# Performance work log

Hardware: AMD Instinct MI355X
Metric: run time of the kernel (lower is better)

## Reference

```python
import jax, jax.numpy as jnp
import numpy as np

LEAK = 0.2
N, C, T, H, DOUT = 512, 16, 15, 32, 32


def setup_inputs() -> dict:
    key = jax.random.key(0)
    k = jax.random.split(key, 5)
    x = jax.random.normal(k[0], (N, C), dtype=jnp.float32)
    adj = jax.random.uniform(k[1], (N, N, T), dtype=jnp.float32)
    W1 = jax.random.normal(k[2], (2 * C, T + 1, H), dtype=jnp.float32) * 0.05
    W2 = jax.random.normal(k[3], (2 * C, T + 1, DOUT), dtype=jnp.float32) * 0.05
    W3 = jax.random.normal(k[4], (C, H), dtype=jnp.float32) * 0.05
    return {"x": x, "adj": adj, "W1": W1, "W2": W2, "W3": W3}


def reference(x, adj, W1, W2, W3):
    n, c = x.shape
    # input_diag: [N,N,C,1], diagonal copy of node features
    diag = jnp.einsum('mn,ni->mni', jnp.eye(n, dtype=x.dtype), x)[..., None]
    # D = concat(adj-weighted broadcast of x, diag) along edge-type axis -> [N,N,C,T+1]
    D = jnp.concatenate([jnp.einsum('mnt,ni->mnit', adj, x), diag], axis=3)
    # symmetrize along channel axis -> [N,N,2C,T+1]
    D = jnp.concatenate([D, jnp.transpose(D, (1, 0, 2, 3))], axis=2)
    K = jnp.einsum('mnit,ith->mnh', D, W1)   # [N,N,H]
    V = jnp.einsum('mnit,itd->mnd', D, W2)   # [N,N,DOUT]
    Q = x @ W3                               # [N,H]
    logits1 = jnp.einsum('nh,nmh->nm', Q, K)
    logits2 = jnp.einsum('mh,nmh->nm', Q, K)
    s1 = jax.nn.softmax(logits1, axis=1)
    s2 = jax.nn.softmax(logits2, axis=0)
    temp = jnp.einsum('nm,nmd->nd', s1, V) + jnp.einsum('nm,nmd->md', s2, V)
    return jnp.maximum(temp, LEAK * temp)  # lrelu
```

## Files before the change

kernel.cpp:

```cpp
#include <hip/hip_runtime.h>
#include <hip/hip_bf16.h>

#define NNODE 512
#define CCH   16
#define TT    15
#define TP    16
#define HH    32
#define DD    32

typedef unsigned short u16;
typedef unsigned int   u32;
typedef short bf8 __attribute__((ext_vector_type(8)));
typedef float f4  __attribute__((ext_vector_type(4)));

__device__ __forceinline__ float bf2f(u16 v) {
    union { u32 u; float f; } x; x.u = ((u32)v) << 16; return x.f;
}
__device__ __forceinline__ u16 f2bf(float f) {
    union { float f; u32 u; } x; x.f = f;
    u32 u = x.u;
    return (u16)((u + 0x7FFFu + ((u >> 16) & 1u)) >> 16);
}
__device__ __forceinline__ void unpack8(uint4 p, float* o) {
    o[0]=bf2f((u16)(p.x & 0xffffu)); o[1]=bf2f((u16)(p.x >> 16));
    o[2]=bf2f((u16)(p.y & 0xffffu)); o[3]=bf2f((u16)(p.y >> 16));
    o[4]=bf2f((u16)(p.z & 0xffffu)); o[5]=bf2f((u16)(p.z >> 16));
    o[6]=bf2f((u16)(p.w & 0xffffu)); o[7]=bf2f((u16)(p.w >> 16));
}
__device__ __forceinline__ uint4 pack8(const u16* v) {
    return make_uint4((u32)v[0]|((u32)v[1]<<16), (u32)v[2]|((u32)v[3]<<16),
                      (u32)v[4]|((u32)v[5]<<16), (u32)v[6]|((u32)v[7]<<16));
}

__global__ __launch_bounds__(256) void k_prep_adjp(
    const float* __restrict__ x, const float* __restrict__ W1,
    const float* __restrict__ W2, const float* __restrict__ W3,
    const float* __restrict__ adj,
    u16* __restrict__ A1, u16* __restrict__ B1,
    u16* __restrict__ A2, u16* __restrict__ B2,
    u16* __restrict__ Qb, float* __restrict__ QAd, float* __restrict__ QB,
    u16* __restrict__ adjP, u16* __restrict__ adjPT)
{
    int tid = threadIdx.x;
    if (blockIdx.x < 512) {
        int n = blockIdx.x;
        __shared__ alignas(16) float xs[CCH];
        __shared__ alignas(16) float A1row[512], B1row[512];
        __shared__ alignas(16) float Qs[HH];
        if (tid < CCH) xs[tid] = x[n*CCH + tid];
        __syncthreads();
        float xr[CCH];
        #pragma unroll
        for (int i=0;i<CCH;i++) xr[i]=xs[i];
        #pragma unroll
        for (int rep=0; rep<2; rep++) {
            int c = tid + rep*256;
            float a1=0.f,b1=0.f,a2=0.f,b2=0.f;
            #pragma unroll
            for (int i=0;i<CCH;i++) {
                a1 += xr[i]*W1[i*512 + c];
                b1 += xr[i]*W1[(CCH+i)*512 + c];
                a2 += xr[i]*W2[i*512 + c];
                b2 += xr[i]*W2[(CCH+i)*512 + c];
            }
            A1[(size_t)n*512 + c]=f2bf(a1); B1[(size_t)n*512 + c]=f2bf(b1);
            A2[(size_t)n*512 + c]=f2bf(a2); B2[(size_t)n*512 + c]=f2bf(b2);
            A1row[c]=a1; B1row[c]=b1;
        }
        if (tid < HH) {
            float q=0.f;
            #pragma unroll
            for (int i=0;i<CCH;i++) q += xr[i]*W3[i*HH + tid];
            Qs[tid]=q; Qb[(size_t)n*HH + tid]=f2bf(q);
        }
        __syncthreads();
        if (tid < TP) {
            float qa=0.f, qb=0.f;
            #pragma unroll
            for (int h=0;h<HH;h++) { qa += Qs[h]*A1row[tid*HH+h]; qb += Qs[h]*B1row[tid*HH+h]; }
            QAd[(size_t)n*TP + tid]=qa; QB[(size_t)n*TP + tid]=qb;
        }
    } else {
        int b = blockIdx.x - 512;
        int n0 = (b >> 4) * 32, m0 = (b & 15) * 32;
        __shared__ alignas(16) u16 s[32*520];
        #pragma unroll
        for (int i = 0; i < 60; i++) {
            int e = tid + i*256;
            int nl = e / 480; int rem = e - nl*480;
            int ml = rem / 15; int t = rem - ml*15;
            float v = adj[((size_t)(n0+nl)*512 + (m0+ml))*TT + t];
            s[nl*520 + ml*16 + t] = f2bf(v);
        }
        #pragma unroll
        for (int i = 0; i < 4; i++) {
            int e = tid + i*256; int nl = e >> 5, ml = e & 31;
            s[nl*520 + ml*16 + 15] = ((n0+nl) == (m0+ml)) ? (u16)0x3F80 : (u16)0;
        }
        __syncthreads();
        #pragma unroll
        for (int i = 0; i < 8; i++) {
            int c = tid + i*256;
            int nl = c >> 6, off = (c & 63) * 8;
            uint4 vv = *(const uint4*)(s + nl*520 + off);
            *(uint4*)(adjP + (size_t)(n0+nl)*8192 + m0*16 + off) = vv;
        }
        #pragma unroll
        for (int i = 0; i < 8; i++) {
            int c = tid + i*256;
            int ml = c >> 6, nlh = c & 63, nl = nlh >> 1, half = nlh & 1;
            uint4 vv = *(const uint4*)(s + nl*520 + ml*16 + half*8);
            *(uint4*)(adjPT + (size_t)(m0+ml)*8192 + (n0+nl)*16 + half*8) = vv;
        }
    }
}

__global__ __launch_bounds__(256) void k_gemmGH(
    const u16* __restrict__ Qb, const u16* __restrict__ A1, const u16* __restrict__ B1,
    const u16* __restrict__ A2, const u16* __restrict__ B2,
    u16* __restrict__ G, u16* __restrict__ H,
    u16* __restrict__ A2T, u16* __restrict__ B2T)
{
    int tid = threadIdx.x;
    int bx = blockIdx.x;
    if (bx < 8192) {
        int wv = tid >> 6, lane = tid & 63;
        int l15 = lane & 15, quad = lane >> 4;
        bool isH = bx >= 4096;
        int w = ((isH ? bx - 4096 : bx) << 2) + wv;
        int rt = w >> 9;
        int ct = w & 511;
        const u16* Bsrc = isH ? B1 : A1;
        u16* Dst = isH ? H : G;
        bf8 afrag = *(const bf8*)(Qb + (size_t)(rt*16 + l15)*32 + quad*8);
        bf8 bfrag = *(const bf8*)(Bsrc + (size_t)ct*512 + l15*32 + quad*8);
        f4 acc = {0.f, 0.f, 0.f, 0.f};
        acc = __builtin_amdgcn_mfma_f32_16x16x32_bf16(afrag, bfrag, acc, 0, 0, 0);
        #pragma unroll
        for (int r = 0; r < 4; r++)
            Dst[(size_t)(rt*16 + quad*4 + r)*8192 + ct*16 + l15] = f2bf(acc[r]);
    } else {
        int b = bx - 8192;
        bool isB = b >= 64;
        const u16* src = isB ? B2 : A2;
        u16* dst = isB ? B2T : A2T;
        int idx = ((b & 63) << 8) + tid;
        int d = idx >> 9, k = idx & 511;
        u16 tmp[16];
        #pragma unroll
        for (int t = 0; t < 16; t++) tmp[t] = src[(size_t)k*512 + t*32 + d];
        uint4* o = (uint4*)(dst + (size_t)d*8192 + k*16);
        o[0] = pack8(tmp); o[1] = pack8(tmp+8);
    }
}

__global__ __launch_bounds__(256) void k_combine(
    const u16* __restrict__ adjP, const u16* __restrict__ adjPT,
    const u16* __restrict__ G, const u16* __restrict__ H,
    const float* __restrict__ QAd, const float* __restrict__ QB,
    float* __restrict__ L1, float* __restrict__ L2T)
{
    int m0 = blockIdx.x*16, n0 = blockIdx.y*16;
    int tid = threadIdx.x, ml = tid & 15, nl = tid >> 4;
    int n = n0 + nl, m = m0 + ml;
    __shared__ alignas(16) float tr[16*17];
    const uint4* pA = (const uint4*)(adjP  + (size_t)n*8192 + m*16);
    const uint4* pT = (const uint4*)(adjPT + (size_t)n*8192 + m*16);
    const uint4* pG = (const uint4*)(G + (size_t)n*8192 + m*16);
    const uint4* pH = (const uint4*)(H + (size_t)m*8192 + n*16);
    float a[16], at[16], g[16], h[16], qa[16], qb[16];
    unpack8(pA[0], a);  unpack8(pA[1], a+8);
    unpack8(pT[0], at); unpack8(pT[1], at+8);
    unpack8(pG[0], g);  unpack8(pG[1], g+8);
    unpack8(pH[0], h);  unpack8(pH[1], h+8);
    #pragma unroll
    for (int q4 = 0; q4 < 4; q4++) {
        float4 va = *(const float4*)(QAd + m*16 + q4*4);
        float4 vb = *(const float4*)(QB  + n*16 + q4*4);
        qa[q4*4+0]=va.x; qa[q4*4+1]=va.y; qa[q4*4+2]=va.z; qa[q4*4+3]=va.w;
        qb[q4*4+0]=vb.x; qb[q4*4+1]=vb.y; qb[q4*4+2]=vb.z; qb[q4*4+3]=vb.w;
    }
    float l1 = 0.f, l2 = 0.f;
    #pragma unroll
    for (int t = 0; t < 16; t++) {
        l1 = fmaf(a[t], g[t],  fmaf(at[t], qb[t], l1));
        l2 = fmaf(a[t], qa[t], fmaf(at[t], h[t],  l2));
    }
    L1[(size_t)n*NNODE + m] = l1;
    tr[ml*17+nl] = l2;
    __syncthreads();
    int r = tid >> 4, c = tid & 15;
    L2T[(size_t)(m0+r)*NNODE + n0+c] = tr[r*17+c];
}

__global__ __launch_bounds__(256) void k_softmax_w(
    const float* __restrict__ L1, const float* __restrict__ L2T,
    const u16* __restrict__ adjP, const u16* __restrict__ adjPT,
    u16* __restrict__ W1c, u16* __restrict__ W2c,
    float* __restrict__ u1, float* __restrict__ v2)
{
    int b = blockIdx.x, tid = threadIdx.x;
    bool first = b < NNODE;
    int j = first ? b : b - NNODE;
    const float* row = first ? (L1 + (size_t)j*NNODE) : (L2T + (size_t)j*NNODE);
    u16* W  = (first ? W1c : W2c) + (size_t)j*8192;
    float* uv = (first ? u1 : v2) + (size_t)j*TP;

    float v0 = row[tid], v1 = row[tid+256];
    float mx = fmaxf(v0, v1);
    #pragma unroll
    for (int o=32; o; o>>=1) mx = fmaxf(mx, __shfl_xor(mx, o, 64));
    __shared__ alignas(16) float red[4], red2[4], ur[4][16];
    int lane = tid & 63, wv = tid >> 6;
    if (!lane) red[wv] = mx;
    __syncthreads();
    mx = fmaxf(fmaxf(red[0],red[1]), fmaxf(red[2],red[3]));
    float e0 = __expf(v0 - mx), e1 = __expf(v1 - mx);
    float sm = e0 + e1;
    #pragma unroll
    for (int o=32; o; o>>=1) sm += __shfl_xor(sm, o, 64);
    if (!lane) red2[wv] = sm;
    __syncthreads();
    float inv = 1.0f / (red2[0]+red2[1]+red2[2]+red2[3]);
    float sa = e0*inv, sb = e1*inv;

    const u16* ap = adjP  + (size_t)j*8192;
    const u16* tp = adjPT + (size_t)j*8192;
    float u[16];
    #pragma unroll
    for (int t=0;t<16;t++) u[t]=0.f;
    #pragma unroll
    for (int half = 0; half < 2; half++) {
        int k = tid + half*256;
        float sv = half ? sb : sa;
        const uint4* p = (const uint4*)(ap + k*16);
        float av[16]; unpack8(p[0], av); unpack8(p[1], av+8);
        u16 o16[16];
        #pragma unroll
        for (int t=0;t<16;t++) o16[t] = f2bf(sv*av[t]);
        uint4* wp = (uint4*)(W + k*16);
        wp[0] = pack8(o16); wp[1] = pack8(o16+8);
        const uint4* q = (const uint4*)(tp + k*16);
        float tv[16]; unpack8(q[0], tv); unpack8(q[1], tv+8);
        #pragma unroll
        for (int t=0;t<16;t++) u[t] = fmaf(sv, tv[t], u[t]);
    }
    #pragma unroll
    for (int t=0;t<16;t++) {
        #pragma unroll
        for (int o=32; o; o>>=1) u[t] += __shfl_xor(u[t], o, 64);
    }
    if (!lane) {
        #pragma unroll
        for (int t=0;t<16;t++) ur[wv][t] = u[t];
    }
    __syncthreads();
    if (tid < 16) uv[tid] = ur[0][tid]+ur[1][tid]+ur[2][tid]+ur[3][tid];
}

__global__ __launch_bounds__(256) void k_gemm2(
    const u16* __restrict__ W1c, const u16* __restrict__ W2c,
    const u16* __restrict__ A2T, const u16* __restrict__ B2T,
    float* __restrict__ tempP)
{
    int tid = threadIdx.x;
    int wv = tid >> 6, lane = tid & 63, l15 = lane & 15, quad = lane >> 4;
    int w = blockIdx.x*4 + wv;
    int kc = w & 15, dt = (w >> 4) & 1, jt = w >> 5;
    size_t aRow = (size_t)(jt*16 + l15)*8192;
    size_t bRow = (size_t)(dt*16 + l15)*8192;
    int kt0 = kc*512 + quad*8;
    f4 acc = {0.f, 0.f, 0.f, 0.f};
    #pragma unroll
    for (int s = 0; s < 16; s++) {
        int kt = kt0 + s*32;
        bf8 aw1 = *(const bf8*)(W1c + aRow + kt);
        bf8 ba2 = *(const bf8*)(A2T + bRow + kt);
        acc = __builtin_amdgcn_mfma_f32_16x16x32_bf16(aw1, ba2, acc, 0, 0, 0);
        bf8 aw2 = *(const bf8*)(W2c + aRow + kt);
        bf8 bb2 = *(const bf8*)(B2T + bRow + kt);
        acc = __builtin_amdgcn_mfma_f32_16x16x32_bf16(aw2, bb2, acc, 0, 0, 0);
    }
    #pragma unroll
    for (int r = 0; r < 4; r++)
        tempP[((size_t)kc*NNODE + jt*16 + quad*4 + r)*DD + dt*16 + l15] = acc[r];
}

__global__ __launch_bounds__(256) void k_final(
    const float* __restrict__ tempP, const float* __restrict__ u1, const float* __restrict__ v2,
    const u16* __restrict__ A2, const u16* __restrict__ B2, float* __restrict__ out)
{
    int j0 = blockIdx.x * 8;
    int tid = threadIdx.x;
    int j = tid >> 5, d = tid & 31;
    int jj = j0 + j;
    float acc = 0.f;
    #pragma unroll
    for (int kc=0;kc<16;kc++) acc += tempP[((size_t)kc*NNODE + jj)*DD + d];
    #pragma unroll
    for (int t=0;t<TP;t++) {
        acc += u1[(size_t)jj*TP + t] * bf2f(B2[(size_t)jj*512 + t*32 + d]);
        acc += v2[(size_t)jj*TP + t] * bf2f(A2[(size_t)jj*512 + t*32 + d]);
    }
    out[(size_t)jj*DD + d] = fmaxf(acc, 0.2f*acc);
}

extern "C" void kernel_launch(void* const* d_in, const int* in_sizes, int n_in,
                              void* d_out, int out_size, void* d_ws, size_t ws_size,
                              hipStream_t stream)
{
    (void)in_sizes; (void)n_in; (void)out_size; (void)ws_size;
    const float* x   = (const float*)d_in[0];
    const float* adj = (const float*)d_in[1];
    const float* W1  = (const float*)d_in[2];
    const float* W2  = (const float*)d_in[3];
    const float* W3  = (const float*)d_in[4];

    char* ws = (char*)d_ws;
    u16*   adjP = (u16*)(ws);
    u16*   adjPT= (u16*)(ws + 0x800000);
    u16*   G    = (u16*)(ws + 0x1000000);
    u16*   H    = (u16*)(ws + 0x1800000);
    u16*   W1c  = (u16*)(ws + 0x2000000);
    u16*   W2c  = (u16*)(ws + 0x2800000);
    u16*   A1   = (u16*)(ws + 0x3000000);
    u16*   B1   = (u16*)(ws + 0x3080000);
    u16*   A2   = (u16*)(ws + 0x3100000);
    u16*   B2   = (u16*)(ws + 0x3180000);
    u16*   A2T  = (u16*)(ws + 0x3200000);
    u16*   B2T  = (u16*)(ws + 0x3280000);
    u16*   Qb   = (u16*)(ws + 0x3300000);
    float* QAd  = (float*)(ws + 0x3310000);
    float* QB   = (float*)(ws + 0x3320000);
    float* u1   = (float*)(ws + 0x3330000);
    float* v2   = (float*)(ws + 0x3340000);
    float* L1   = (float*)(ws + 0x3400000);
    float* L2T  = (float*)(ws + 0x3500000);
    float* tempP= (float*)(ws + 0x3600000);

    k_prep_adjp<<<768, 256, 0, stream>>>(x, W1, W2, W3, adj,
                                         A1, B1, A2, B2, Qb, QAd, QB, adjP, adjPT);
    k_gemmGH<<<8320, 256, 0, stream>>>(Qb, A1, B1, A2, B2, G, H, A2T, B2T);
    k_combine<<<dim3(32,32), 256, 0, stream>>>(adjP, adjPT, G, H, QAd, QB, L1, L2T);
    k_softmax_w<<<1024, 256, 0, stream>>>(L1, L2T, adjP, adjPT, W1c, W2c, u1, v2);
    k_gemm2<<<256, 256, 0, stream>>>(W1c, W2c, A2T, B2T, tempP);
    k_final<<<64, 256, 0, stream>>>(tempP, u1, v2, A2, B2, (float*)d_out);
}
```

Baseline: 120.6 us.

## Fuse G/H MFMA into logits kernel and move A2/B2 transpose into prep

The G and H intermediates (each 8 MB of bf16) are no longer materialised. Each logits block now recomputes its needed Q·A1 and Q·B1 tiles with MFMA and contracts them on the fly against adjP/adjPT, reducing across lanes with shuffles. The A2/B2 transposes move into the prep kernel, which drops a whole launch and the G/H global write and read traffic. In exchange there are redundant MFMA recomputations per block, scattered 2-byte adjacency loads instead of vectorised 32-byte loads, and shuffle reductions.

```diff
diff --git a/kernel.cpp b/kernel.cpp
--- a/kernel.cpp
+++ b/kernel.cpp
@@ -38,6 +38,7 @@
     const float* __restrict__ adj,
     u16* __restrict__ A1, u16* __restrict__ B1,
     u16* __restrict__ A2, u16* __restrict__ B2,
+    u16* __restrict__ A2T, u16* __restrict__ B2T,
     u16* __restrict__ Qb, float* __restrict__ QAd, float* __restrict__ QB,
     u16* __restrict__ adjP, u16* __restrict__ adjPT)
 {
@@ -46,6 +47,7 @@
         int n = blockIdx.x;
         __shared__ alignas(16) float xs[CCH];
         __shared__ alignas(16) float A1row[512], B1row[512];
+        __shared__ alignas(16) float A2row[512], B2row[512];
         __shared__ alignas(16) float Qs[HH];
         if (tid < CCH) xs[tid] = x[n*CCH + tid];
         __syncthreads();
@@ -65,7 +67,7 @@
             }
             A1[(size_t)n*512 + c]=f2bf(a1); B1[(size_t)n*512 + c]=f2bf(b1);
             A2[(size_t)n*512 + c]=f2bf(a2); B2[(size_t)n*512 + c]=f2bf(b2);
-            A1row[c]=a1; B1row[c]=b1;
+            A1row[c]=a1; B1row[c]=b1; A2row[c]=a2; B2row[c]=b2;
         }
         if (tid < HH) {
             float q=0.f;
@@ -79,6 +81,13 @@
             #pragma unroll
             for (int h=0;h<HH;h++) { qa += Qs[h]*A1row[tid*HH+h]; qb += Qs[h]*B1row[tid*HH+h]; }
             QAd[(size_t)n*TP + tid]=qa; QB[(size_t)n*TP + tid]=qb;
+        }
+        {
+            int d = tid >> 3, t0 = (tid & 7) * 2;
+            u32 pa = (u32)f2bf(A2row[t0*32 + d]) | ((u32)f2bf(A2row[(t0+1)*32 + d]) << 16);
+            u32 pb = (u32)f2bf(B2row[t0*32 + d]) | ((u32)f2bf(B2row[(t0+1)*32 + d]) << 16);
+            *(u32*)(A2T + (size_t)d*8192 + n*16 + t0) = pa;
+            *(u32*)(B2T + (size_t)d*8192 + n*16 + t0) = pb;
         }
     } else {
         int b = blockIdx.x - 512;
@@ -115,82 +124,65 @@
     }
 }
 
-__global__ __launch_bounds__(256) void k_gemmGH(
+__global__ __launch_bounds__(256) void k_logits(
     const u16* __restrict__ Qb, const u16* __restrict__ A1, const u16* __restrict__ B1,
-    const u16* __restrict__ A2, const u16* __restrict__ B2,
-    u16* __restrict__ G, u16* __restrict__ H,
-    u16* __restrict__ A2T, u16* __restrict__ B2T)
-{
-    int tid = threadIdx.x;
-    int bx = blockIdx.x;
-    if (bx < 8192) {
-        int wv = tid >> 6, lane = tid & 63;
-        int l15 = lane & 15, quad = lane >> 4;
-        bool isH = bx >= 4096;
-        int w = ((isH ? bx - 4096 : bx) << 2) + wv;
-        int rt = w >> 9;
-        int ct = w & 511;
-        const u16* Bsrc = isH ? B1 : A1;
-        u16* Dst = isH ? H : G;
-        bf8 afrag = *(const bf8*)(Qb + (size_t)(rt*16 + l15)*32 + quad*8);
-        bf8 bfrag = *(const bf8*)(Bsrc + (size_t)ct*512 + l15*32 + quad*8);
-        f4 acc = {0.f, 0.f, 0.f, 0.f};
-        acc = __builtin_amdgcn_mfma_f32_16x16x32_bf16(afrag, bfrag, acc, 0, 0, 0);
-        #pragma unroll
-        for (int r = 0; r < 4; r++)
-            Dst[(size_t)(rt*16 + quad*4 + r)*8192 + ct*16 + l15] = f2bf(acc[r]);
-    } else {
-        int b = bx - 8192;
-        bool isB = b >= 64;
-        const u16* src = isB ? B2 : A2;
-        u16* dst = isB ? B2T : A2T;
-        int idx = ((b & 63) << 8) + tid;
-        int d = idx >> 9, k = idx & 511;
-        u16 tmp[16];
-        #pragma unroll
-        for (int t = 0; t < 16; t++) tmp[t] = src[(size_t)k*512 + t*32 + d];
-        uint4* o = (uint4*)(dst + (size_t)d*8192 + k*16);
-        o[0] = pack8(tmp); o[1] = pack8(tmp+8);
-    }
-}
-
-__global__ __launch_bounds__(256) void k_combine(
     const u16* __restrict__ adjP, const u16* __restrict__ adjPT,
-    const u16* __restrict__ G, const u16* __restrict__ H,
     const float* __restrict__ QAd, const float* __restrict__ QB,
     float* __restrict__ L1, float* __restrict__ L2T)
 {
-    int m0 = blockIdx.x*16, n0 = blockIdx.y*16;
-    int tid = threadIdx.x, ml = tid & 15, nl = tid >> 4;
-    int n = n0 + nl, m = m0 + ml;
-    __shared__ alignas(16) float tr[16*17];
-    const uint4* pA = (const uint4*)(adjP  + (size_t)n*8192 + m*16);
-    const uint4* pT = (const uint4*)(adjPT + (size_t)n*8192 + m*16);
-    const uint4* pG = (const uint4*)(G + (size_t)n*8192 + m*16);
-    const uint4* pH = (const uint4*)(H + (size_t)m*8192 + n*16);
-    float a[16], at[16], g[16], h[16], qa[16], qb[16];
-    unpack8(pA[0], a);  unpack8(pA[1], a+8);
-    unpack8(pT[0], at); unpack8(pT[1], at+8);
-    unpack8(pG[0], g);  unpack8(pG[1], g+8);
-    unpack8(pH[0], h);  unpack8(pH[1], h+8);
-    #pragma unroll
-    for (int q4 = 0; q4 < 4; q4++) {
-        float4 va = *(const float4*)(QAd + m*16 + q4*4);
-        float4 vb = *(const float4*)(QB  + n*16 + q4*4);
-        qa[q4*4+0]=va.x; qa[q4*4+1]=va.y; qa[q4*4+2]=va.z; qa[q4*4+3]=va.w;
-        qb[q4*4+0]=vb.x; qb[q4*4+1]=vb.y; qb[q4*4+2]=vb.z; qb[q4*4+3]=vb.w;
-    }
-    float l1 = 0.f, l2 = 0.f;
-    #pragma unroll
-    for (int t = 0; t < 16; t++) {
-        l1 = fmaf(a[t], g[t],  fmaf(at[t], qb[t], l1));
-        l2 = fmaf(a[t], qa[t], fmaf(at[t], h[t],  l2));
-    }
-    L1[(size_t)n*NNODE + m] = l1;
-    tr[ml*17+nl] = l2;
+    const int m0 = blockIdx.x * 16, n0 = blockIdx.y * 16;
+    const int tid = threadIdx.x;
+    const int wv = tid >> 6, lane = tid & 63, l15 = lane & 15, quad = lane >> 4;
+    __shared__ alignas(16) float sL1[16*17];
+    __shared__ alignas(16) float sL2[16*17];
+
+    bf8 afragN = *(const bf8*)(Qb + (size_t)(n0 + l15)*32 + quad*8);
+    bf8 afragM = *(const bf8*)(Qb + (size_t)(m0 + l15)*32 + quad*8);
+
+    f4 accG[4], accH[4];
+    #pragma unroll
+    for (int j = 0; j < 4; j++) {
+        int m = m0 + wv*4 + j;
+        int n = n0 + wv*4 + j;
+        bf8 bG = *(const bf8*)(A1 + (size_t)m*512 + l15*32 + quad*8);
+        bf8 bH = *(const bf8*)(B1 + (size_t)n*512 + l15*32 + quad*8);
+        f4 z = {0.f,0.f,0.f,0.f};
+        accG[j] = __builtin_amdgcn_mfma_f32_16x16x32_bf16(afragN, bG, z, 0, 0, 0);
+        accH[j] = __builtin_amdgcn_mfma_f32_16x16x32_bf16(afragM, bH, z, 0, 0, 0);
+    }
+
+    #pragma unroll
+    for (int j = 0; j < 4; j++) {
+        int m = m0 + wv*4 + j;
+        #pragma unroll
+        for (int r = 0; r < 4; r++) {
+            int n = n0 + quad*4 + r;
+            float a  = bf2f(adjP [(size_t)n*8192 + m*16 + l15]);
+            float at = bf2f(adjPT[(size_t)n*8192 + m*16 + l15]);
+            float v = a*accG[j][r] + at*QB[n*16 + l15];
+            #pragma unroll
+            for (int o = 1; o < 16; o <<= 1) v += __shfl_xor(v, o, 64);
+            if (l15 == 0) sL1[(quad*4+r)*17 + wv*4 + j] = v;
+        }
+    }
+    #pragma unroll
+    for (int j = 0; j < 4; j++) {
+        int n = n0 + wv*4 + j;
+        #pragma unroll
+        for (int r = 0; r < 4; r++) {
+            int m = m0 + quad*4 + r;
+            float a  = bf2f(adjP [(size_t)n*8192 + m*16 + l15]);
+            float at = bf2f(adjPT[(size_t)n*8192 + m*16 + l15]);
+            float v = a*QAd[m*16 + l15] + at*accH[j][r];
+            #pragma unroll
+            for (int o = 1; o < 16; o <<= 1) v += __shfl_xor(v, o, 64);
+            if (l15 == 0) sL2[(quad*4+r)*17 + wv*4 + j] = v;
+        }
+    }
     __syncthreads();
-    int r = tid >> 4, c = tid & 15;
-    L2T[(size_t)(m0+r)*NNODE + n0+c] = tr[r*17+c];
+    int row = tid >> 4, col = tid & 15;
+    L1 [(size_t)(n0+row)*NNODE + m0 + col] = sL1[row*17+col];
+    L2T[(size_t)(m0+row)*NNODE + n0 + col] = sL2[row*17+col];
 }
 
 __global__ __launch_bounds__(256) void k_softmax_w(
@@ -319,29 +311,26 @@
     char* ws = (char*)d_ws;
     u16*   adjP = (u16*)(ws);
     u16*   adjPT= (u16*)(ws + 0x800000);
-    u16*   G    = (u16*)(ws + 0x1000000);
-    u16*   H    = (u16*)(ws + 0x1800000);
-    u16*   W1c  = (u16*)(ws + 0x2000000);
-    u16*   W2c  = (u16*)(ws + 0x2800000);
-    u16*   A1   = (u16*)(ws + 0x3000000);
-    u16*   B1   = (u16*)(ws + 0x3080000);
-    u16*   A2   = (u16*)(ws + 0x3100000);
-    u16*   B2   = (u16*)(ws + 0x3180000);
-    u16*   A2T  = (u16*)(ws + 0x3200000);
-    u16*   B2T  = (u16*)(ws + 0x3280000);
-    u16*   Qb   = (u16*)(ws + 0x3300000);
-    float* QAd  = (float*)(ws + 0x3310000);
-    float* QB   = (float*)(ws + 0x3320000);
-    float* u1   = (float*)(ws + 0x3330000);
-    float* v2   = (float*)(ws + 0x3340000);
-    float* L1   = (float*)(ws + 0x3400000);
-    float* L2T  = (float*)(ws + 0x3500000);
-    float* tempP= (float*)(ws + 0x3600000);
+    u16*   W1c  = (u16*)(ws + 0x1000000);
+    u16*   W2c  = (u16*)(ws + 0x1800000);
+    u16*   A1   = (u16*)(ws + 0x2000000);
+    u16*   B1   = (u16*)(ws + 0x2080000);
+    u16*   A2   = (u16*)(ws + 0x2100000);
+    u16*   B2   = (u16*)(ws + 0x2180000);
+    u16*   A2T  = (u16*)(ws + 0x2200000);
+    u16*   B2T  = (u16*)(ws + 0x2280000);
+    u16*   Qb   = (u16*)(ws + 0x2300000);
+    float* QAd  = (float*)(ws + 0x2310000);
+    float* QB   = (float*)(ws + 0x2320000);
+    float* u1   = (float*)(ws + 0x2330000);
+    float* v2   = (float*)(ws + 0x2340000);
+    float* L1   = (float*)(ws + 0x2400000);
+    float* L2T  = (float*)(ws + 0x2500000);
+    float* tempP= (float*)(ws + 0x2600000);
 
     k_prep_adjp<<<768, 256, 0, stream>>>(x, W1, W2, W3, adj,
-                                         A1, B1, A2, B2, Qb, QAd, QB, adjP, adjPT);
-    k_gemmGH<<<8320, 256, 0, stream>>>(Qb, A1, B1, A2, B2, G, H, A2T, B2T);
-    k_combine<<<dim3(32,32), 256, 0, stream>>>(adjP, adjPT, G, H, QAd, QB, L1, L2T);
+                                         A1, B1, A2, B2, A2T, B2T, Qb, QAd, QB, adjP, adjPT);
+    k_logits<<<dim3(32,32), 256, 0, stream>>>(Qb, A1, B1, adjP, adjPT, QAd, QB, L1, L2T);
     k_softmax_w<<<1024, 256, 0, stream>>>(L1, L2T, adjP, adjPT, W1c, W2c, u1, v2);
     k_gemm2<<<256, 256, 0, stream>>>(W1c, W2c, A2T, B2T, tempP);
     k_final<<<64, 256, 0, stream>>>(tempP, u1, v2, A2, B2, (float*)d_out);
```

After: 115.5 us. 4.2% less time.
